# Performance work log

Hardware: AMD Instinct MI355X
Metric: run time of the kernel (lower is better)

Reference implementation:

```python
import jax, jax.numpy as jnp
import numpy as np

V, E, H, L = 32000, 512, 512, 3
HI = 2 * H  # expansion_factor = 2
B, S = 16, 2048


def setup_inputs() -> dict:
    key = jax.random.key(0)
    ks = jax.random.split(key, 9)
    x_source = jax.random.randint(ks[0], (B, S), 1, V)
    x_lengths = jax.random.randint(ks[1], (B,), 1, S + 1)
    x_lengths = x_lengths.at[0].set(S)  # ensure max(x_lengths) == S so truncation is static
    emb = jax.random.normal(ks[2], (V, E), jnp.float32) * 0.02
    emb = emb.at[0].set(0.0)  # padding_idx=0
    W_er = jax.random.normal(ks[3], (E, H), jnp.float32) / np.sqrt(E)
    b_er = jnp.zeros((H,), jnp.float32)
    W_hg_fwd = jax.random.normal(ks[4], (L, H, 2 * HI), jnp.float32) / np.sqrt(H)
    W_out_fwd = jax.random.normal(ks[5], (L, HI, H), jnp.float32) / np.sqrt(HI)
    W_hg_rev = jax.random.normal(ks[6], (L, H, 2 * HI), jnp.float32) / np.sqrt(H)
    W_out_rev = jax.random.normal(ks[7], (L, HI, H), jnp.float32) / np.sqrt(HI)
    return {"x_source": x_source, "x_lengths": x_lengths, "emb": emb,
            "W_er": W_er, "b_er": b_er,
            "W_hg_fwd": W_hg_fwd, "W_out_fwd": W_out_fwd,
            "W_hg_rev": W_hg_rev, "W_out_rev": W_out_rev}


def _log_g(x):
    # log of g(x) = where(x>=0, x+0.5, sigmoid(x)), computed stably in log space
    return jnp.where(x >= 0, jnp.log(jax.nn.relu(x) + 0.5), -jax.nn.softplus(-x))


def _mingru(x, W_hg, W_out):
    # x: [B,S,H] -> [B,S,H]; parallel minGRU via Heinsen associative scan in log space
    hidden, gate = jnp.split(x @ W_hg, 2, axis=-1)  # each [B,S,HI]
    log_coeffs = -jax.nn.softplus(gate)             # log(1 - z)
    log_values = -jax.nn.softplus(-gate) + _log_g(hidden)  # log z + log g(h~)
    a_star = jnp.cumsum(log_coeffs, axis=1)
    log_h = a_star + jax.lax.cumlogsumexp(log_values - a_star, axis=1)
    return jnp.exp(log_h) @ W_out


def _circ_shift_left(x, pad):
    # per-sample left rotation by pad[i]: cat([x[i, pad:], x[i, :pad]])
    Sl = x.shape[1]
    idx = (jnp.arange(Sl)[None, :] + pad[:, None]) % Sl  # [B,S]
    return jnp.take_along_axis(x, idx[:, :, None], axis=1)


def reference(x_source, x_lengths, emb, W_er, b_er, W_hg_fwd, W_out_fwd, W_hg_rev, W_out_rev):
    # seq_length = max(x_lengths) == S by construction, so truncation is identity
    x_emb = emb[x_source] @ W_er + b_er            # [B,S,H]
    pad = x_emb.shape[1] - x_lengths               # [B]
    rev = _circ_shift_left(jnp.flip(x_emb, axis=1), pad)
    h, hr = x_emb, rev
    for i in range(W_hg_fwd.shape[0]):
        h = _mingru(h, W_hg_fwd[i], W_out_fwd[i])
        hr = _mingru(hr, W_hg_rev[i], W_out_rev[i])
    hr = _circ_shift_left(jnp.flip(hr, axis=1), pad)
    out = jnp.concatenate([h, hr], axis=-1)        # [B,S,2H]
    # flattened gather in original == out[i, x_lengths[i]-1]
    seq_h = out[jnp.arange(out.shape[0]), x_lengths - 1]  # [B,2H]
    return out, seq_h
```

## Files before the change

kernel.cpp:

```cpp
#include <hip/hip_runtime.h>
#include <hip/hip_bf16.h>
#include <stdint.h>

#define S_LEN  2048
#define BATCH  16
#define HDIM   512
#define HIDIM  1024
#define NLAYER 3
#define SCAN_C 32
#define SCAN_T 64

typedef __hip_bfloat16 bf16;
typedef __attribute__((ext_vector_type(8))) short bf16x8;
typedef __attribute__((ext_vector_type(4))) float f32x4;
typedef unsigned int u32;

#define GLOAD16(gp, lp) __builtin_amdgcn_global_load_lds(                 \
    (const __attribute__((address_space(1))) void*)(gp),                  \
    (__attribute__((address_space(3))) void*)(lp), 16, 0, 0)

__global__ void probe_dtype(const unsigned short* __restrict__ w, int* __restrict__ flag)
{
  int cnt = 0;
  for (int i = threadIdx.x; i < 4096; i += 64) {
    unsigned short m = w[i] & 0x7FFF;
    if (m > 0x4080) cnt++;
  }
  for (int o = 32; o; o >>= 1) cnt += __shfl_down(cnt, o, 64);
  if (threadIdx.x == 0) *flag = (cnt > 64) ? 1 : 0;
}

__device__ __forceinline__ void av_calc(float hid, float gate, float& a, float& v) {
  a = 1.0f / (1.0f + __expf(gate));
  float z = 1.0f / (1.0f + __expf(-gate));
  float g = (hid >= 0.0f) ? (hid + 0.5f) : (1.0f / (1.0f + __expf(-hid)));
  v = z * g;
}

__device__ __forceinline__ short f2bs(float f) {
  bf16 h = (bf16)f;
  return *(short*)&h;
}

__device__ __forceinline__ bf16x8 pack8(float4 a, float4 b) {
  bf16x8 r;
  r[0] = f2bs(a.x); r[1] = f2bs(a.y); r[2] = f2bs(a.z); r[3] = f2bs(a.w);
  r[4] = f2bs(b.x); r[5] = f2bs(b.y); r[6] = f2bs(b.z); r[7] = f2bs(b.w);
  return r;
}

__global__ __launch_bounds__(256, 3)
void gemm_lds(const bf16* __restrict__ A, const bf16* __restrict__ Bt,
              bf16* __restrict__ Cout, int K, int lda, int ldc)
{
  __shared__ bf16 As[128 * 32];
  __shared__ bf16 Bs[128 * 32];

  const int tid  = threadIdx.x;
  const int wave = tid >> 6;
  const int lane = tid & 63;

  const u32 nwg = gridDim.x * gridDim.y;
  const u32 hb  = blockIdx.y * gridDim.x + blockIdx.x;
  const u32 cpx = nwg >> 3;
  const u32 swz = (hb & 7u) * cpx + (hb >> 3);
  const int m0 = (int)(swz / gridDim.x) * 128;
  const int n0 = (int)(swz % gridDim.x) * 128;

  const int srow = wave * 32 + (lane >> 2);
  const int sk   = (lane & 3) * 8;
  const bf16* gA0 = A  + (long)(m0 + srow) * lda + sk;
  const bf16* gA1 = gA0 + 16 * (long)lda;
  const bf16* gB0 = Bt + (long)(n0 + srow) * K + sk;
  const bf16* gB1 = gB0 + 16 * (long)K;
  bf16* lA0 = &As[(wave * 2 + 0) * 512];
  bf16* lA1 = &As[(wave * 2 + 1) * 512];
  bf16* lB0 = &Bs[(wave * 2 + 0) * 512];
  bf16* lB1 = &Bs[(wave * 2 + 1) * 512];

  f32x4 acc[4][4];
#pragma unroll
  for (int i = 0; i < 4; i++)
#pragma unroll
    for (int j = 0; j < 4; j++)
#pragma unroll
      for (int r = 0; r < 4; r++) acc[i][j][r] = 0.0f;

  const int mBase = (wave >> 1) * 64;
  const int nBase = (wave & 1) * 64;
  const int fr = lane & 15;
  const int fq = (lane >> 4) * 8;

  for (int k0 = 0; k0 < K; k0 += 32) {
    GLOAD16(gA0, lA0);
    GLOAD16(gA1, lA1);
    GLOAD16(gB0, lB0);
    GLOAD16(gB1, lB1);
    gA0 += 32; gA1 += 32; gB0 += 32; gB1 += 32;
    __syncthreads();

    bf16x8 afr[4], bfr[4];
#pragma unroll
    for (int mt = 0; mt < 4; mt++)
      afr[mt] = *(const bf16x8*)&As[(mBase + mt * 16 + fr) * 32 + fq];
#pragma unroll
    for (int nt = 0; nt < 4; nt++)
      bfr[nt] = *(const bf16x8*)&Bs[(nBase + nt * 16 + fr) * 32 + fq];

#pragma unroll
    for (int mt = 0; mt < 4; mt++)
#pragma unroll
      for (int nt = 0; nt < 4; nt++)
        acc[mt][nt] = __builtin_amdgcn_mfma_f32_16x16x32_bf16(afr[mt], bfr[nt], acc[mt][nt], 0, 0, 0);

    __syncthreads();
  }

  const int orow = (lane >> 4) * 4;
  const int ocol = lane & 15;
#pragma unroll
  for (int mt = 0; mt < 4; mt++) {
#pragma unroll
    for (int nt = 0; nt < 4; nt++) {
      int gr = m0 + mBase + mt * 16 + orow;
      int gc = n0 + nBase + nt * 16 + ocol;
#pragma unroll
      for (int r = 0; r < 4; r++)
        Cout[(long)(gr + r) * ldc + gc] = (bf16)acc[mt][nt][r];
    }
  }
}

template<int GATHER, int BIAS>
__global__ __launch_bounds__(256, 2)
void gemm_mfma(const void* __restrict__ Av, const bf16* __restrict__ Bt,
               bf16* __restrict__ Cout, const float* __restrict__ bias,
               const int* __restrict__ gidx, const int* __restrict__ flag,
               int M, int N, int K, int lda, int ldc)
{
  __shared__ bf16 As[128 * 32];
  __shared__ bf16 Bs[128 * 32];

  const int tid  = threadIdx.x;
  const int wave = tid >> 6;
  const int lane = tid & 63;
  const int m0 = blockIdx.y * 128;
  const int n0 = blockIdx.x * 128;

  const int seg0 = wave * 2, seg1 = seg0 + 1;
  const int lr = lane >> 2;
  const int ck = (lane & 3) * 8;
  const int rA0 = seg0 * 16 + lr;
  const int rA1 = seg1 * 16 + lr;

  const int af = GATHER ? *flag : 0;

  long ga0 = GATHER ? (long)gidx[m0 + rA0] : (long)(m0 + rA0);
  long ga1 = GATHER ? (long)gidx[m0 + rA1] : (long)(m0 + rA1);
  const bf16*  hA0 = (const bf16*)Av + ga0 * (long)lda + ck;
  const bf16*  hA1 = (const bf16*)Av + ga1 * (long)lda + ck;
  const float* qA0 = (const float*)Av + ga0 * (long)lda + ck;
  const float* qA1 = (const float*)Av + ga1 * (long)lda + ck;
  const bf16*  pB0 = Bt + (long)(n0 + rA0) * K + ck;
  const bf16*  pB1 = Bt + (long)(n0 + rA1) * K + ck;

  bf16* lA0 = &As[seg0 * 512 + lane * 8];
  bf16* lA1 = &As[seg1 * 512 + lane * 8];
  bf16* lB0 = &Bs[seg0 * 512 + lane * 8];
  bf16* lB1 = &Bs[seg1 * 512 + lane * 8];

  f32x4 acc[4][4];
#pragma unroll
  for (int i = 0; i < 4; i++)
#pragma unroll
    for (int j = 0; j < 4; j++)
#pragma unroll
      for (int r = 0; r < 4; r++) acc[i][j][r] = 0.0f;

  const int mBase = (wave >> 1) * 64;
  const int nBase = (wave & 1) * 64;
  const int fr = lane & 15;
  const int fq = (lane >> 4) * 8;

  for (int k0 = 0; k0 < K; k0 += 32) {
    bf16x8 va0, va1;
    if (GATHER && af) {
      float4 a0 = *(const float4*)(qA0 + k0);
      float4 a1 = *(const float4*)(qA0 + k0 + 4);
      float4 b0 = *(const float4*)(qA1 + k0);
      float4 b1 = *(const float4*)(qA1 + k0 + 4);
      va0 = pack8(a0, a1);
      va1 = pack8(b0, b1);
    } else {
      va0 = *(const bf16x8*)(hA0 + k0);
      va1 = *(const bf16x8*)(hA1 + k0);
    }
    bf16x8 vb0 = *(const bf16x8*)(pB0 + k0);
    bf16x8 vb1 = *(const bf16x8*)(pB1 + k0);
    __syncthreads();
    *(bf16x8*)lA0 = va0;
    *(bf16x8*)lA1 = va1;
    *(bf16x8*)lB0 = vb0;
    *(bf16x8*)lB1 = vb1;
    __syncthreads();

    bf16x8 afr[4], bfr[4];
#pragma unroll
    for (int mt = 0; mt < 4; mt++)
      afr[mt] = *(const bf16x8*)&As[(mBase + mt * 16 + fr) * 32 + fq];
#pragma unroll
    for (int nt = 0; nt < 4; nt++)
      bfr[nt] = *(const bf16x8*)&Bs[(nBase + nt * 16 + fr) * 32 + fq];

#pragma unroll
    for (int mt = 0; mt < 4; mt++)
#pragma unroll
      for (int nt = 0; nt < 4; nt++)
        acc[mt][nt] = __builtin_amdgcn_mfma_f32_16x16x32_bf16(afr[mt], bfr[nt], acc[mt][nt], 0, 0, 0);
  }

  const int orow = (lane >> 4) * 4;
  const int ocol = lane & 15;
#pragma unroll
  for (int mt = 0; mt < 4; mt++) {
#pragma unroll
    for (int nt = 0; nt < 4; nt++) {
      int gr = m0 + mBase + mt * 16 + orow;
      int gc = n0 + nBase + nt * 16 + ocol;
      float bv = BIAS ? bias[gc] : 0.0f;
#pragma unroll
      for (int r = 0; r < 4; r++) {
        float v = acc[mt][nt][r] + bv;
        Cout[(long)(gr + r) * ldc + gc] = (bf16)v;
      }
    }
  }
}

__global__ __launch_bounds__(256)
void transpose_conv(const void* __restrict__ in, bf16* __restrict__ out,
                    const int* __restrict__ flag, int R, int C)
{
  __shared__ float tile[32][33];
  int f = *flag;
  int x = blockIdx.x * 32 + threadIdx.x;
  int yb = blockIdx.y * 32;
#pragma unroll
  for (int i = threadIdx.y; i < 32; i += 8) {
    long idx = (long)(yb + i) * C + x;
    tile[i][threadIdx.x] = f ? ((const float*)in)[idx] : (float)((const bf16*)in)[idx];
  }
  __syncthreads();
  int x2 = yb + threadIdx.x;
  int y2b = blockIdx.x * 32;
#pragma unroll
  for (int i = threadIdx.y; i < 32; i += 8)
    out[(long)(y2b + i) * R + x2] = (bf16)tile[threadIdx.x][i];
}

__global__ __launch_bounds__(256)
void transpose_conv2(const void* __restrict__ in32, const void* __restrict__ in16,
                     bf16* __restrict__ out, const int* __restrict__ flag, int R, int C)
{
  __shared__ float tile[32][33];
  int f = *flag;
  int x = blockIdx.x * 32 + threadIdx.x;
  int yb = blockIdx.y * 32;
#pragma unroll
  for (int i = threadIdx.y; i < 32; i += 8) {
    long idx = (long)(yb + i) * C + x;
    tile[i][threadIdx.x] = f ? ((const float*)in32)[idx] : (float)((const bf16*)in16)[idx];
  }
  __syncthreads();
  int x2 = yb + threadIdx.x;
  int y2b = blockIdx.x * 32;
#pragma unroll
  for (int i = threadIdx.y; i < 32; i += 8)
    out[(long)(y2b + i) * R + x2] = (bf16)tile[threadIdx.x][i];
}

__global__ __launch_bounds__(256)
void conv_to_f32(const void* __restrict__ in, float* __restrict__ out,
                 const int* __restrict__ flag, int n)
{
  int i = blockIdx.x * blockDim.x + threadIdx.x;
  if (i >= n) return;
  out[i] = (*flag) ? ((const float*)in)[i] : (float)((const bf16*)in)[i];
}

__global__ __launch_bounds__(256)
void scan_pass1(const bf16* __restrict__ HG, float* __restrict__ Ab, float* __restrict__ Pb)
{
  int tid = blockIdx.x * blockDim.x + threadIdx.x;
  int c  = tid & (HIDIM - 1);
  int bj = tid >> 10;
  int j  = bj & (SCAN_C - 1);
  int b  = bj >> 5;
  const bf16* base = HG + ((long)(b * S_LEN + j * SCAN_T)) * 2048 + c;
  float A = 1.0f, P = 0.0f;
#pragma unroll 4
  for (int t = 0; t < SCAN_T; t++) {
    float hid = (float)base[(long)t * 2048];
    float gt  = (float)base[(long)t * 2048 + 1024];
    float a, v; av_calc(hid, gt, a, v);
    A *= a;
    P = fmaf(a, P, v);
  }
  Ab[tid] = A;
  Pb[tid] = P;
}

__global__ __launch_bounds__(256)
void scan_pass2(const float* __restrict__ Ab, float* __restrict__ Pb)
{
  int tid = blockIdx.x * blockDim.x + threadIdx.x;
  int c = tid & (HIDIM - 1);
  int b = tid >> 10;
  float h = 0.0f;
  for (int j = 0; j < SCAN_C; j++) {
    long i = ((long)(b * SCAN_C + j) << 10) + c;
    float A = Ab[i];
    float P = Pb[i];
    Pb[i] = h;
    h = fmaf(A, h, P);
  }
}

__global__ __launch_bounds__(256)
void scan_pass3(bf16* __restrict__ HG, const float* __restrict__ Pb)
{
  int tid = blockIdx.x * blockDim.x + threadIdx.x;
  int c  = tid & (HIDIM - 1);
  int bj = tid >> 10;
  int j  = bj & (SCAN_C - 1);
  int b  = bj >> 5;
  bf16* base = HG + ((long)(b * S_LEN + j * SCAN_T)) * 2048 + c;
  float h = Pb[tid];
#pragma unroll 4
  for (int t = 0; t < SCAN_T; t++) {
    float hid = (float)base[(long)t * 2048];
    float gt  = (float)base[(long)t * 2048 + 1024];
    float a, v; av_calc(hid, gt, a, v);
    h = fmaf(a, h, v);
    base[(long)t * 2048] = (bf16)h;
  }
}

__global__ __launch_bounds__(256)
void rev_build(const bf16* __restrict__ X, bf16* __restrict__ X2, const int* __restrict__ lens)
{
  int bt = blockIdx.x;
  int b = bt >> 11;
  int t = bt & (S_LEN - 1);
  int pad = S_LEN - lens[b];
  int src = S_LEN - 1 - ((t + pad) & (S_LEN - 1));
  const u32* s = (const u32*)(X + (long)(b * S_LEN + src) * HDIM);
  u32* d = (u32*)(X2 + (long)(b * S_LEN + t) * HDIM);
  d[threadIdx.x] = s[threadIdx.x];
}

__global__ __launch_bounds__(256)
void finalize_out(const bf16* __restrict__ X, const bf16* __restrict__ X2,
                  const int* __restrict__ lens, const int* __restrict__ flag,
                  void* __restrict__ out)
{
  int bt = blockIdx.x;
  int b = bt >> 11;
  int t = bt & (S_LEN - 1);
  int pad = S_LEN - lens[b];
  int src = S_LEN - 1 - ((t + pad) & (S_LEN - 1));
  const bf16* sf = X  + (long)(b * S_LEN + t) * HDIM;
  const bf16* sr = X2 + (long)(b * S_LEN + src) * HDIM;
  long ro = (long)(b * S_LEN + t) * 1024;
  if (*flag) {
    float* d = (float*)out + ro;
    for (int c = threadIdx.x; c < 512; c += 256) {
      d[c]       = (float)sf[c];
      d[512 + c] = (float)sr[c];
    }
  } else {
    bf16* d = (bf16*)out + ro;
    for (int c = threadIdx.x; c < 512; c += 256) {
      d[c]       = sf[c];
      d[512 + c] = sr[c];
    }
  }
}

__global__ __launch_bounds__(256)
void seq_out_k(const bf16* __restrict__ X, const bf16* __restrict__ X2,
               const int* __restrict__ lens, const int* __restrict__ flag,
               void* __restrict__ out)
{
  int b = blockIdx.x;
  int t = lens[b] - 1;
  const bf16* sf = X  + (long)(b * S_LEN + t) * HDIM;
  const bf16* sr = X2 + (long)(b * S_LEN + 0) * HDIM;
  long off = (long)BATCH * S_LEN * 1024 + (long)b * 1024;
  if (*flag) {
    float* d = (float*)out + off;
    for (int c = threadIdx.x; c < 512; c += 256) {
      d[c]       = (float)sf[c];
      d[512 + c] = (float)sr[c];
    }
  } else {
    bf16* d = (bf16*)out + off;
    for (int c = threadIdx.x; c < 512; c += 256) {
      d[c]       = sf[c];
      d[512 + c] = sr[c];
    }
  }
}

extern "C" void kernel_launch(void* const* d_in, const int* in_sizes, int n_in,
                              void* d_out, int out_size, void* d_ws, size_t ws_size,
                              hipStream_t stream)
{
  (void)in_sizes; (void)n_in; (void)out_size;
  const int* x_source = (const int*)d_in[0];
  const int* x_len    = (const int*)d_in[1];
  const void* emb     = d_in[2];
  const void* W_er    = d_in[3];
  const void* b_er    = d_in[4];
  const void* W_hg[2]  = { d_in[5], d_in[7] };
  const void* W_out[2] = { d_in[6], d_in[8] };

  char* ws = (char*)d_ws;
  size_t off = 0;
  auto alloc = [&](size_t bytes) -> char* {
    char* p = ws + off;
    off += (bytes + 255) & ~(size_t)255;
    return p;
  };
  auto a256 = [](size_t b) -> size_t { return (b + 255) & ~(size_t)255; };

  int*   flag = (int*)  alloc(256);
  float* berF = (float*)alloc(512 * 4);
  bf16*  WerT = (bf16*) alloc((size_t)512 * 512 * 2);
  bf16*  X    = (bf16*) alloc((size_t)BATCH * S_LEN * HDIM * 2);
  bf16*  X2   = (bf16*) alloc((size_t)BATCH * S_LEN * HDIM * 2);
  bf16* WhgT[2][NLAYER];
  bf16* WoutT[2][NLAYER];
  for (int d = 0; d < 2; d++)
    for (int l = 0; l < NLAYER; l++) {
      WhgT[d][l]  = (bf16*)alloc((size_t)2048 * 512 * 2);
      WoutT[d][l] = (bf16*)alloc((size_t)512 * 1024 * 2);
    }

  size_t fixedEnd = off;
  int bch = 16;
  while (bch > 1) {
    size_t need = fixedEnd
      + a256((size_t)bch * S_LEN * 2048 * 2)
      + 2 * a256((size_t)bch * SCAN_C * HIDIM * 4);
    if (need <= ws_size) break;
    bch >>= 1;
  }
  bf16*  HG = (bf16*) alloc((size_t)bch * S_LEN * 2048 * 2);
  float* Ab = (float*)alloc((size_t)bch * SCAN_C * HIDIM * 4);
  float* Pb = (float*)alloc((size_t)bch * SCAN_C * HIDIM * 4);

  probe_dtype<<<1, 64, 0, stream>>>((const unsigned short*)emb, flag);

  conv_to_f32<<<2, 256, 0, stream>>>(b_er, berF, flag, 512);
  dim3 tb(32, 8);
  transpose_conv<<<dim3(16, 16), tb, 0, stream>>>(W_er, WerT, flag, 512, 512);
  for (int d = 0; d < 2; d++)
    for (int l = 0; l < NLAYER; l++) {
      const char* hg32 = (const char*)W_hg[d] + (size_t)l * 512 * 2048 * 4;
      const char* hg16 = (const char*)W_hg[d] + (size_t)l * 512 * 2048 * 2;
      const char* wo32 = (const char*)W_out[d] + (size_t)l * 1024 * 512 * 4;
      const char* wo16 = (const char*)W_out[d] + (size_t)l * 1024 * 512 * 2;
      transpose_conv2<<<dim3(2048 / 32, 512 / 32), tb, 0, stream>>>(hg32, hg16, WhgT[d][l], flag, 512, 2048);
      transpose_conv2<<<dim3(512 / 32, 1024 / 32), tb, 0, stream>>>(wo32, wo16, WoutT[d][l], flag, 1024, 512);
    }

  gemm_mfma<1, 1><<<dim3(4, (BATCH * S_LEN) / 128), 256, 0, stream>>>(
      emb, WerT, X, berF, x_source, flag, BATCH * S_LEN, 512, 512, 512, 512);

  rev_build<<<BATCH * S_LEN, 256, 0, stream>>>(X, X2, x_len);

  for (int d = 0; d < 2; d++) {
    bf16* Xd = d ? X2 : X;
    for (int l = 0; l < NLAYER; l++) {
      for (int cb = 0; cb < BATCH / bch; cb++) {
        bf16* Ain = Xd + (size_t)cb * bch * S_LEN * HDIM;
        int Mrows = bch * S_LEN;
        gemm_lds<<<dim3(16, Mrows / 128), 256, 0, stream>>>(
            Ain, WhgT[d][l], HG, 512, 512, 2048);
        int nthr = bch * SCAN_C * HIDIM;
        scan_pass1<<<nthr / 256, 256, 0, stream>>>(HG, Ab, Pb);
        scan_pass2<<<(bch * HIDIM) / 256, 256, 0, stream>>>(Ab, Pb);
        scan_pass3<<<nthr / 256, 256, 0, stream>>>(HG, Pb);
        gemm_lds<<<dim3(4, Mrows / 128), 256, 0, stream>>>(
            HG, WoutT[d][l], Ain, 1024, 2048, 512);
      }
    }
  }

  finalize_out<<<BATCH * S_LEN, 256, 0, stream>>>(X, X2, x_len, flag, d_out);
  seq_out_k<<<BATCH, 256, 0, stream>>>(X, X2, x_len, flag, d_out);
}
```

Measured before the change: 1.794 ms.

## Replace GEMM with 256x256-tile double-buffered LDS pipeline using 8 waves

Replaces the 128x128, 4-wave GEMM used for both minGRU projections with a 256x256-tile kernel that has 8 waves and 128 KB of dynamic LDS. The kernel double-buffers A and B tiles in 64-wide K halves with XOR-swizzled LDS addressing. Global-to-LDS loads for the next stage are interleaved with MFMA quarters, paced by explicit vmcnt waits and barriers, and s_setprio raises priority during the MFMA bursts. The aim is more data reuse per tile, less LDS bank conflict and overlap of memory traffic with compute. In exchange it needs a very large LDS allocation, which limits occupancy to one block per CU, and coarser tiles mean fewer blocks for the narrower output GEMM.

Result: no change. 1.777 ms (-0.9%).

```diff
diff --git a/kernel.cpp b/kernel.cpp
--- a/kernel.cpp
+++ b/kernel.cpp
@@ -19,6 +19,10 @@
     (const __attribute__((address_space(1))) void*)(gp),                  \
     (__attribute__((address_space(3))) void*)(lp), 16, 0, 0)
 
+#define FENCE asm volatile("" ::: "memory")
+#define BAR   do { FENCE; __builtin_amdgcn_s_barrier(); FENCE; } while (0)
+#define VMCNT(n) asm volatile("s_waitcnt vmcnt(" #n ")" ::: "memory")
+
 __global__ void probe_dtype(const unsigned short* __restrict__ w, int* __restrict__ flag)
 {
   int cnt = 0;
@@ -49,83 +53,171 @@
   return r;
 }
 
-__global__ __launch_bounds__(256, 3)
-void gemm_lds(const bf16* __restrict__ A, const bf16* __restrict__ Bt,
-              bf16* __restrict__ Cout, int K, int lda, int ldc)
-{
-  __shared__ bf16 As[128 * 32];
-  __shared__ bf16 Bs[128 * 32];
+
+__device__ __forceinline__ void stage_half(const bf16* __restrict__ G, int row0, int ld,
+                                           int kbase, char* lhalf, int tid)
+{
+  const int r  = tid >> 3;
+  const int cc = (((tid & 7) ^ ((tid >> 3) & 7)) << 3);
+  const bf16* g0 = G + (long)(row0 + r) * ld + (kbase + cc);
+  char* l = lhalf + ((tid >> 6) << 10);
+  GLOAD16(g0, l);
+  GLOAD16(g0 + (long)64 * ld, l + 8192);
+}
+
+__device__ __forceinline__ bf16x8 frag_ld(const char* base, int Rl, int cb) {
+  return *(const bf16x8*)(base + Rl * 128 + (cb ^ ((Rl & 7) << 4)));
+}
+
+__global__ __launch_bounds__(512, 2)
+void gemm8(const bf16* __restrict__ A, const bf16* __restrict__ Bt,
+           bf16* __restrict__ Cout, int K, int lda, int ldc)
+{
+  extern __shared__ char lds[];
 
   const int tid  = threadIdx.x;
   const int wave = tid >> 6;
   const int lane = tid & 63;
+  const int wm = wave >> 2;
+  const int wn = wave & 3;
 
   const u32 nwg = gridDim.x * gridDim.y;
   const u32 hb  = blockIdx.y * gridDim.x + blockIdx.x;
   const u32 cpx = nwg >> 3;
   const u32 swz = (hb & 7u) * cpx + (hb >> 3);
-  const int m0 = (int)(swz / gridDim.x) * 128;
-  const int n0 = (int)(swz % gridDim.x) * 128;
-
-  const int srow = wave * 32 + (lane >> 2);
-  const int sk   = (lane & 3) * 8;
-  const bf16* gA0 = A  + (long)(m0 + srow) * lda + sk;
-  const bf16* gA1 = gA0 + 16 * (long)lda;
-  const bf16* gB0 = Bt + (long)(n0 + srow) * K + sk;
-  const bf16* gB1 = gB0 + 16 * (long)K;
-  bf16* lA0 = &As[(wave * 2 + 0) * 512];
-  bf16* lA1 = &As[(wave * 2 + 1) * 512];
-  bf16* lB0 = &Bs[(wave * 2 + 0) * 512];
-  bf16* lB1 = &Bs[(wave * 2 + 1) * 512];
-
-  f32x4 acc[4][4];
-#pragma unroll
-  for (int i = 0; i < 4; i++)
+  const int m0 = (int)(swz / gridDim.x) * 256;
+  const int n0 = (int)(swz % gridDim.x) * 256;
+
+  char* A0 = lds;
+  char* B0 = lds + 32768;
+  char* A1 = lds + 65536;
+  char* B1 = lds + 98304;
+
+  const int fr = lane & 15;
+  const int qh = lane >> 4;
+  const int cqh = qh * 16;
+
+  f32x4 acc[8][4];
+#pragma unroll
+  for (int i = 0; i < 8; i++)
 #pragma unroll
     for (int j = 0; j < 4; j++)
 #pragma unroll
       for (int r = 0; r < 4; r++) acc[i][j][r] = 0.0f;
 
-  const int mBase = (wave >> 1) * 64;
-  const int nBase = (wave & 1) * 64;
-  const int fr = lane & 15;
-  const int fq = (lane >> 4) * 8;
-
-  for (int k0 = 0; k0 < K; k0 += 32) {
-    GLOAD16(gA0, lA0);
-    GLOAD16(gA1, lA1);
-    GLOAD16(gB0, lB0);
-    GLOAD16(gB1, lB1);
-    gA0 += 32; gA1 += 32; gB0 += 32; gB1 += 32;
-    __syncthreads();
-
-    bf16x8 afr[4], bfr[4];
-#pragma unroll
-    for (int mt = 0; mt < 4; mt++)
-      afr[mt] = *(const bf16x8*)&As[(mBase + mt * 16 + fr) * 32 + fq];
-#pragma unroll
-    for (int nt = 0; nt < 4; nt++)
-      bfr[nt] = *(const bf16x8*)&Bs[(nBase + nt * 16 + fr) * 32 + fq];
-
-#pragma unroll
-    for (int mt = 0; mt < 4; mt++)
-#pragma unroll
-      for (int nt = 0; nt < 4; nt++)
-        acc[mt][nt] = __builtin_amdgcn_mfma_f32_16x16x32_bf16(afr[mt], bfr[nt], acc[mt][nt], 0, 0, 0);
-
-    __syncthreads();
-  }
-
-  const int orow = (lane >> 4) * 4;
-  const int ocol = lane & 15;
-#pragma unroll
-  for (int mt = 0; mt < 4; mt++) {
-#pragma unroll
-    for (int nt = 0; nt < 4; nt++) {
-      int gr = m0 + mBase + mt * 16 + orow;
-      int gc = n0 + nBase + nt * 16 + ocol;
-#pragma unroll
-      for (int r = 0; r < 4; r++)
+  const int NJ = K >> 7;
+
+  stage_half(A,  m0,       lda, 0,  A0,         tid);
+  stage_half(A,  m0 + 128, lda, 0,  A0 + 16384, tid);
+  stage_half(Bt, n0,       K,   0,  B0,         tid);
+  stage_half(Bt, n0 + 128, K,   0,  B0 + 16384, tid);
+  stage_half(Bt, n0,       K,   64, B1,         tid);
+  stage_half(Bt, n0 + 128, K,   64, B1 + 16384, tid);
+  VMCNT(4);
+  BAR;
+
+  for (int j = 0; j < NJ; ++j) {
+    const int last = (j == NJ - 1);
+    const int kO  = (2 * j + 1) * 64;
+    const int kE2 = (2 * j + 2) * 64;
+    const int kO2 = (2 * j + 3) * 64;
+
+    {
+      bf16x8 bfrag[4][2];
+#pragma unroll
+      for (int q = 0; q < 4; ++q) {
+        if (q == 0) {
+#pragma unroll
+          for (int nt = 0; nt < 4; ++nt)
+#pragma unroll
+            for (int kk = 0; kk < 2; ++kk)
+              bfrag[nt][kk] = frag_ld(B0, wn * 64 + nt * 16 + fr, kk * 64 + cqh);
+        }
+        bf16x8 afrag[2][2];
+#pragma unroll
+        for (int t = 0; t < 2; ++t)
+#pragma unroll
+          for (int kk = 0; kk < 2; ++kk)
+            afrag[t][kk] = frag_ld(A0, wm * 128 + (2 * q + t) * 16 + fr, kk * 64 + cqh);
+
+        if (q == 0) {
+          stage_half(A, m0,       lda, kO, A1,         tid);
+          stage_half(A, m0 + 128, lda, kO, A1 + 16384, tid);
+        } else if (q == 1) {
+          if (!last) stage_half(Bt, n0,       K, kE2, B0,         tid);
+        } else if (q == 2) {
+          if (!last) stage_half(Bt, n0 + 128, K, kE2, B0 + 16384, tid);
+        }
+
+        BAR;
+        __builtin_amdgcn_s_setprio(1);
+#pragma unroll
+        for (int t = 0; t < 2; ++t)
+#pragma unroll
+          for (int nt = 0; nt < 4; ++nt)
+#pragma unroll
+            for (int kk = 0; kk < 2; ++kk)
+              acc[2 * q + t][nt] = __builtin_amdgcn_mfma_f32_16x16x32_bf16(
+                  afrag[t][kk], bfrag[nt][kk], acc[2 * q + t][nt], 0, 0, 0);
+        __builtin_amdgcn_s_setprio(0);
+        if (q == 3) {
+          if (last) { VMCNT(0); } else { VMCNT(4); }
+        }
+        BAR;
+      }
+    }
+
+    {
+      bf16x8 bfrag[4][2];
+#pragma unroll
+      for (int q = 0; q < 4; ++q) {
+        if (q == 0) {
+#pragma unroll
+          for (int nt = 0; nt < 4; ++nt)
+#pragma unroll
+            for (int kk = 0; kk < 2; ++kk)
+              bfrag[nt][kk] = frag_ld(B1, wn * 64 + nt * 16 + fr, kk * 64 + cqh);
+        }
+        bf16x8 afrag[2][2];
+#pragma unroll
+        for (int t = 0; t < 2; ++t)
+#pragma unroll
+          for (int kk = 0; kk < 2; ++kk)
+            afrag[t][kk] = frag_ld(A1, wm * 128 + (2 * q + t) * 16 + fr, kk * 64 + cqh);
+
+        if (!last) {
+          if (q == 0)      stage_half(A,  m0,       lda, kE2, A0,         tid);
+          else if (q == 1) stage_half(A,  m0 + 128, lda, kE2, A0 + 16384, tid);
+          else if (q == 2) stage_half(Bt, n0,       K,   kO2, B1,         tid);
+          else             stage_half(Bt, n0 + 128, K,   kO2, B1 + 16384, tid);
+        }
+
+        BAR;
+        __builtin_amdgcn_s_setprio(1);
+#pragma unroll
+        for (int t = 0; t < 2; ++t)
+#pragma unroll
+          for (int nt = 0; nt < 4; ++nt)
+#pragma unroll
+            for (int kk = 0; kk < 2; ++kk)
+              acc[2 * q + t][nt] = __builtin_amdgcn_mfma_f32_16x16x32_bf16(
+                  afrag[t][kk], bfrag[nt][kk], acc[2 * q + t][nt], 0, 0, 0);
+        __builtin_amdgcn_s_setprio(0);
+        if (q == 3 && !last) { VMCNT(4); }
+        BAR;
+      }
+    }
+  }
+
+  const int orow = qh * 4;
+#pragma unroll
+  for (int mt = 0; mt < 8; ++mt) {
+#pragma unroll
+    for (int nt = 0; nt < 4; ++nt) {
+      int gr = m0 + wm * 128 + mt * 16 + orow;
+      int gc = n0 + wn * 64 + nt * 16 + fr;
+#pragma unroll
+      for (int r = 0; r < 4; ++r)
         Cout[(long)(gr + r) * ldc + gc] = (bf16)acc[mt][nt][r];
     }
   }
@@ -486,13 +578,13 @@
       for (int cb = 0; cb < BATCH / bch; cb++) {
         bf16* Ain = Xd + (size_t)cb * bch * S_LEN * HDIM;
         int Mrows = bch * S_LEN;
-        gemm_lds<<<dim3(16, Mrows / 128), 256, 0, stream>>>(
+        gemm8<<<dim3(2048 / 256, Mrows / 256), 512, 131072, stream>>>(
             Ain, WhgT[d][l], HG, 512, 512, 2048);
         int nthr = bch * SCAN_C * HIDIM;
         scan_pass1<<<nthr / 256, 256, 0, stream>>>(HG, Ab, Pb);
         scan_pass2<<<(bch * HIDIM) / 256, 256, 0, stream>>>(Ab, Pb);
         scan_pass3<<<nthr / 256, 256, 0, stream>>>(HG, Pb);
-        gemm_lds<<<dim3(4, Mrows / 128), 256, 0, stream>>>(
+        gemm8<<<dim3(512 / 256, Mrows / 256), 512, 131072, stream>>>(
             HG, WoutT[d][l], Ain, 1024, 2048, 512);
       }
     }
```
